# Optimization experiments

Measured on AMD Instinct MI355X. Metric: run time of the kernel, lower is better.

## Reference

```python
import jax, jax.numpy as jnp
import numpy as np

N, E, G = 50000, 800000, 64
IN, HID, H1, H2, OUT = 128, 64, 4, 4, 10
NEG_SLOPE = 0.2


def gat_layer(h, src, dst, W, attn_l, attn_r, bias, n_nodes, n_heads, d):
    # h: [N, F_in] -> feat: [N, H, D]
    feat = (h @ W).reshape(n_nodes, n_heads, d)
    el = jnp.sum(feat * attn_l, axis=-1)          # [N, H]
    er = jnp.sum(feat * attn_r, axis=-1)          # [N, H]
    e = jax.nn.leaky_relu(el[src] + er[dst], NEG_SLOPE)  # [E, H]
    # edge softmax per destination node (numerically stable)
    m = jax.ops.segment_max(e, dst, num_segments=n_nodes)   # [N, H]
    ex = jnp.exp(e - m[dst])                                 # [E, H]
    s = jax.ops.segment_sum(ex, dst, num_segments=n_nodes)   # [N, H]
    alpha = ex / s[dst]                                      # [E, H]
    msg = alpha[:, :, None] * feat[src]                      # [E, H, D]
    out = jax.ops.segment_sum(msg, dst, num_segments=n_nodes)  # [N, H, D]
    return jax.nn.elu(out + bias.reshape(1, n_heads, d))


def setup_inputs() -> dict:
    key = jax.random.key(0)
    ks = jax.random.split(key, 16)
    x = jax.random.normal(ks[0], (N, IN), dtype=jnp.float32)
    src = jax.random.randint(ks[1], (E,), 0, N, dtype=jnp.int32)
    dst = jax.random.randint(ks[2], (E,), 0, N, dtype=jnp.int32)
    graph_ids = jnp.sort(jax.random.randint(ks[3], (N,), 0, G, dtype=jnp.int32))
    sc1 = 1.0 / np.sqrt(IN)
    sc2 = 1.0 / np.sqrt(HID * H1)
    W1 = jax.random.normal(ks[4], (IN, H1 * HID), dtype=jnp.float32) * sc1
    attn_l1 = jax.random.normal(ks[5], (H1, HID), dtype=jnp.float32) * 0.1
    attn_r1 = jax.random.normal(ks[6], (H1, HID), dtype=jnp.float32) * 0.1
    b1 = jnp.zeros((H1 * HID,), dtype=jnp.float32)
    W2 = jax.random.normal(ks[7], (H1 * HID, H2 * HID), dtype=jnp.float32) * sc2
    attn_l2 = jax.random.normal(ks[8], (H2, HID), dtype=jnp.float32) * 0.1
    attn_r2 = jax.random.normal(ks[9], (H2, HID), dtype=jnp.float32) * 0.1
    b2 = jnp.zeros((H2 * HID,), dtype=jnp.float32)
    fcW = jax.random.normal(ks[10], (HID, OUT), dtype=jnp.float32) * (1.0 / np.sqrt(HID))
    fcb = jnp.zeros((OUT,), dtype=jnp.float32)
    return {"x": x, "src": src, "dst": dst, "graph_ids": graph_ids,
            "W1": W1, "attn_l1": attn_l1, "attn_r1": attn_r1, "b1": b1,
            "W2": W2, "attn_l2": attn_l2, "attn_r2": attn_r2, "b2": b2,
            "fcW": fcW, "fcb": fcb}


def reference(x, src, dst, graph_ids, W1, attn_l1, attn_r1, b1,
              W2, attn_l2, attn_r2, b2, fcW, fcb):
    h = gat_layer(x, src, dst, W1, attn_l1, attn_r1, b1, N, H1, HID)
    h = h.reshape(N, H1 * HID)                    # flatten heads (layer 0)
    h = gat_layer(h, src, dst, W2, attn_l2, attn_r2, b2, N, H2, HID)
    h = h.mean(axis=1)                            # mean over heads (layer 1) -> [N, HID]
    pooled = jax.ops.segment_sum(h, graph_ids, num_segments=G)  # SumPooling -> [G, HID]
    return pooled @ fcW + fcb                     # dropout is identity in eval
```

## Files before the change

kernel.cpp:

```cpp
#include <hip/hip_runtime.h>
#include <math.h>

#define NN 50000
#define MPAD 50048
#define NE 800000
#define NG 64
#define FIN 128
#define FH 256
#define HID 64
#define NH 4
#define NOUT 10
#define NEG_SLOPE 0.2f
#define NSB ((NN + 1023) / 1024)

typedef unsigned short u16;
typedef __attribute__((ext_vector_type(8))) short short8;
typedef __attribute__((ext_vector_type(4))) float f32x4;

static __device__ __forceinline__ float leaky(float x){ return x > 0.f ? x : NEG_SLOPE * x; }
static __device__ __forceinline__ float elu1(float x){ return x > 0.f ? x : (__expf(x) - 1.f); }
static __device__ __forceinline__ float b2f(u16 u){
  union { unsigned int i; float f; } v; v.i = ((unsigned)u) << 16; return v.f;
}
static __device__ __forceinline__ u16 f2b(float f){
  union { float f; unsigned int i; } v; v.f = f;
  unsigned r = v.i + 0x7FFFu + ((v.i >> 16) & 1u);
  return (u16)(r >> 16);
}

static __device__ __forceinline__ void gl_lds16(const u16* g, u16* l){
  __builtin_amdgcn_global_load_lds(
      (const __attribute__((address_space(1))) void*)g,
      (__attribute__((address_space(3))) void*)l, 16, 0, 0);
}

#define HIST_BLKS ((NE + 255) / 256)
#define F2B_BLKS (NN * FIN / 4 / 256)
#define W1_BLKS  (FIN * FH / 256)
#define W2_BLKS  (FH * FH / 256)
__global__ void k_histprep(const int* __restrict__ dst, int* __restrict__ cnt,
                           int* __restrict__ rank,
                           const float* __restrict__ x, u16* __restrict__ xh,
                           const float* __restrict__ W1, u16* __restrict__ Wtc1,
                           const float* __restrict__ W2, u16* __restrict__ Wtc2,
                           float* __restrict__ pooled)
{
  int b = blockIdx.x;
  if (b < HIST_BLKS){
    int i = b * 256 + threadIdx.x;
    if (i < NE) rank[i] = atomicAdd(&cnt[dst[i]], 1);
  } else if (b < HIST_BLKS + F2B_BLKS){
    int i = ((b - HIST_BLKS) * 256 + threadIdx.x) * 4;
    float4 v = *reinterpret_cast<const float4*>(x + i);
    ushort4 o; o.x = f2b(v.x); o.y = f2b(v.y); o.z = f2b(v.z); o.w = f2b(v.w);
    *reinterpret_cast<ushort4*>(xh + i) = o;
  } else if (b < HIST_BLKS + F2B_BLKS + W1_BLKS){
    int e = (b - HIST_BLKS - F2B_BLKS) * 256 + threadIdx.x;
    int k = e >> 8, c = e & 255;
    float w = W1[e];
    u16 hi = f2b(w);
    float lo = w - b2f(hi);
    Wtc1[(size_t)c * 2 * FIN + k] = hi;
    Wtc1[(size_t)c * 2 * FIN + FIN + k] = f2b(lo);
  } else if (b < HIST_BLKS + F2B_BLKS + W1_BLKS + W2_BLKS){
    int e = (b - HIST_BLKS - F2B_BLKS - W1_BLKS) * 256 + threadIdx.x;
    int k = e >> 8, c = e & 255;
    float w = W2[e];
    u16 hi = f2b(w);
    float lo = w - b2f(hi);
    Wtc2[(size_t)c * 2 * FH + k] = hi;
    Wtc2[(size_t)c * 2 * FH + FH + k] = f2b(lo);
  } else {
    float4 z = make_float4(0.f, 0.f, 0.f, 0.f);
    #pragma unroll
    for (int l = 0; l < 4; l++)
      *reinterpret_cast<float4*>(pooled + (l * 256 + threadIdx.x) * 4) = z;
  }
}

__global__ __launch_bounds__(256) void k_scan1(const int* __restrict__ cnt,
    int* __restrict__ offs, int* __restrict__ bsum)
{
  __shared__ int wsum[4];
  int t = threadIdx.x;
  int lane = t & 63, wv = t >> 6;
  int base = blockIdx.x * 1024 + t * 4;
  int4 v = make_int4(0, 0, 0, 0);
  if (base + 3 < NN) v = *reinterpret_cast<const int4*>(cnt + base);
  else {
    if (base + 0 < NN) v.x = cnt[base + 0];
    if (base + 1 < NN) v.y = cnt[base + 1];
    if (base + 2 < NN) v.z = cnt[base + 2];
  }
  int s = v.x + v.y + v.z + v.w;
  int incl = s;
  #pragma unroll
  for (int d = 1; d < 64; d <<= 1){
    int u = __shfl_up(incl, d);
    if (lane >= d) incl += u;
  }
  if (lane == 63) wsum[wv] = incl;
  __syncthreads();
  int woff = 0;
  #pragma unroll
  for (int i = 0; i < 4; i++) if (i < wv) woff += wsum[i];
  int texcl = woff + incl - s;
  int e0 = texcl, e1 = e0 + v.x, e2 = e1 + v.y, e3 = e2 + v.z;
  if (base + 3 < NN) *reinterpret_cast<int4*>(offs + base) = make_int4(e0, e1, e2, e3);
  else {
    if (base + 0 < NN) offs[base + 0] = e0;
    if (base + 1 < NN) offs[base + 1] = e1;
    if (base + 2 < NN) offs[base + 2] = e2;
  }
  if (t == 255) bsum[blockIdx.x] = woff + incl;
}

__global__ void k_scan2(const int* __restrict__ bsum, int* __restrict__ bpre)
{
  int lane = threadIdx.x;
  int s = (lane < NSB) ? bsum[lane] : 0;
  int incl = s;
  #pragma unroll
  for (int d = 1; d < 64; d <<= 1){
    int u = __shfl_up(incl, d);
    if (lane >= d) incl += u;
  }
  if (lane < NSB) bpre[lane] = incl - s;
}

__global__ void k_scatter(const int* __restrict__ src, const int* __restrict__ dst,
                          const int* __restrict__ offs, const int* __restrict__ bpre,
                          const int* __restrict__ rank, int* __restrict__ csrc){
  int i = blockIdx.x * blockDim.x + threadIdx.x;
  if (i < NE){
    int d = dst[i];
    csrc[offs[d] + bpre[d >> 10] + rank[i]] = src[i];
  }
}

template<int K>
__global__ __launch_bounds__(512) void k_gemm_bf(
    const u16* __restrict__ A, const u16* __restrict__ Wtc, u16* __restrict__ C,
    const float* __restrict__ attn_l, const float* __restrict__ attn_r,
    float* __restrict__ el, float* __restrict__ er)
{
  constexpr int K2 = 2 * K;
  __shared__ union {
    struct { u16 a[128 * 32]; u16 b[256 * 32]; } s;
    u16 ct[128 * 256];
  } L;
  int t = threadIdx.x;
  int wv = t >> 6, lane = t & 63;
  int row0 = blockIdx.x * 128;
  int lr = lane & 15, lk = lane >> 4;
  int wm = wv >> 2, wn = wv & 3;

  f32x4 acc[4][4];
  #pragma unroll
  for (int m = 0; m < 4; m++)
    #pragma unroll
    for (int n = 0; n < 4; n++) acc[m][n] = (f32x4){0.f, 0.f, 0.f, 0.f};

  const u16* asrc = A + (size_t)(row0 + wv * 16 + (lane >> 2)) * K + (lane & 3) * 8;
  u16* aldst = &L.s.a[wv * 512];
  const u16* bsrc0 = Wtc + (size_t)(wv * 32 + (lane >> 2)) * K2 + (lane & 3) * 8;
  const u16* bsrc1 = Wtc + (size_t)(wv * 32 + 16 + (lane >> 2)) * K2 + (lane & 3) * 8;
  u16* bldst0 = &L.s.b[wv * 1024];
  u16* bldst1 = &L.s.b[wv * 1024 + 512];

  for (int k0 = 0; k0 < K2; k0 += 32){
    int acol = k0 & (K - 1);
    gl_lds16(asrc + acol, aldst);
    gl_lds16(bsrc0 + k0, bldst0);
    gl_lds16(bsrc1 + k0, bldst1);
    __syncthreads();
    short8 af[4], bf[4];
    #pragma unroll
    for (int m = 0; m < 4; m++)
      af[m] = *reinterpret_cast<const short8*>(&L.s.a[(wm * 64 + m * 16 + lr) * 32 + lk * 8]);
    #pragma unroll
    for (int n = 0; n < 4; n++)
      bf[n] = *reinterpret_cast<const short8*>(&L.s.b[(wn * 64 + n * 16 + lr) * 32 + lk * 8]);
    #pragma unroll
    for (int m = 0; m < 4; m++)
      #pragma unroll
      for (int n = 0; n < 4; n++)
        acc[m][n] = __builtin_amdgcn_mfma_f32_16x16x32_bf16(af[m], bf[n], acc[m][n], 0, 0, 0);
    __syncthreads();
  }

  int rg = lane >> 4;
  #pragma unroll
  for (int m = 0; m < 4; m++)
    #pragma unroll
    for (int n = 0; n < 4; n++)
      #pragma unroll
      for (int r = 0; r < 4; r++)
        L.ct[(wm * 64 + m * 16 + rg * 4 + r) * 256 + wn * 64 + n * 16 + lr] = f2b(acc[m][n][r]);
  __syncthreads();
  #pragma unroll
  for (int l = 0; l < 8; l++){
    int idx = t + l * 512;
    int row = idx >> 5, colg = idx & 31;
    short8 v = *reinterpret_cast<const short8*>(&L.ct[row * 256 + colg * 8]);
    *reinterpret_cast<short8*>(C + (size_t)(row0 + row) * 256 + colg * 8) = v;
  }

  {
    int r = t >> 2, hh = t & 3;
    const u16* crow = &L.ct[r * 256 + hh * 64];
    float pl = 0.f, pr = 0.f;
    #pragma unroll
    for (int d8 = 0; d8 < 8; d8++){
      short8 cv = *reinterpret_cast<const short8*>(crow + d8 * 8);
      const float* alp = &attn_l[hh * 64 + d8 * 8];
      const float* arp = &attn_r[hh * 64 + d8 * 8];
      #pragma unroll
      for (int q = 0; q < 8; q++){
        float fv = b2f((u16)cv[q]);
        pl = fmaf(fv, alp[q], pl);
        pr = fmaf(fv, arp[q], pr);
      }
    }
    int orow = row0 + r;
    el[orow * 4 + hh] = pl;
    er[orow * 4 + hh] = pr;
  }
}

template<int LAYER>
__global__ __launch_bounds__(256) void k_agg2(const u16* __restrict__ feat,
    const float* __restrict__ el, const float* __restrict__ er,
    const int* __restrict__ offs, const int* __restrict__ bpre,
    const int* __restrict__ cnt, const int* __restrict__ csrc,
    const float* __restrict__ bias, void* __restrict__ outv)
{
  int wv = threadIdx.x >> 6, lane = threadIdx.x & 63;
  int n = blockIdx.x * 4 + wv;
  if (n >= NN) return;
  int e0 = offs[n] + bpre[n >> 10];
  int deg = cnt[n];
  int hs = lane & 3, slot = lane >> 2;
  int ha = lane >> 4;
  float erh = er[n * 4 + hs];

  float m = -1e30f, srun = 0.f;
  float a0 = 0.f, a1 = 0.f, a2 = 0.f, a3 = 0.f;

  for (int base = 0; base < deg; base += 16){
    int cntc = min(16, deg - base);
    int idx = base + slot;
    int sj = 0; float v = -1e30f;
    if (idx < deg){
      sj = csrc[e0 + idx];
      v = leaky(el[sj * 4 + hs] + erh);
    }
    float cmax = v;
    #pragma unroll
    for (int d = 4; d < 64; d <<= 1) cmax = fmaxf(cmax, __shfl_xor(cmax, d));
    float nm = fmaxf(m, cmax);
    float fac = __expf(m - nm);
    float ex = __expf(v - nm);
    float csum = ex;
    #pragma unroll
    for (int d = 4; d < 64; d <<= 1) csum += __shfl_xor(csum, d);
    srun = srun * fac + csum;
    m = nm;
    float fa = __shfl(fac, ha);
    a0 *= fa; a1 *= fa; a2 *= fa; a3 *= fa;
    #pragma unroll 4
    for (int jj = 0; jj < cntc; jj++){
      float w = __shfl(ex, jj * 4 + ha);
      int sjj = __shfl(sj, jj * 4);
      ushort4 fv = *reinterpret_cast<const ushort4*>(feat + (size_t)sjj * FH + lane * 4);
      a0 = fmaf(w, b2f(fv.x), a0);
      a1 = fmaf(w, b2f(fv.y), a1);
      a2 = fmaf(w, b2f(fv.z), a2);
      a3 = fmaf(w, b2f(fv.w), a3);
    }
  }

  float invh = (deg > 0) ? 1.f / srun : 0.f;
  float inv = __shfl(invh, ha);
  float4 bv = *reinterpret_cast<const float4*>(&bias[lane * 4]);
  a0 = elu1(a0 * inv + bv.x); a1 = elu1(a1 * inv + bv.y);
  a2 = elu1(a2 * inv + bv.z); a3 = elu1(a3 * inv + bv.w);

  if (LAYER == 1){
    u16* out = (u16*)outv;
    ushort4 o; o.x = f2b(a0); o.y = f2b(a1); o.z = f2b(a2); o.w = f2b(a3);
    *reinterpret_cast<ushort4*>(out + (size_t)n * FH + lane * 4) = o;
  } else {
    float* out = (float*)outv;
    a0 += __shfl_xor(a0, 16); a0 += __shfl_xor(a0, 32);
    a1 += __shfl_xor(a1, 16); a1 += __shfl_xor(a1, 32);
    a2 += __shfl_xor(a2, 16); a2 += __shfl_xor(a2, 32);
    a3 += __shfl_xor(a3, 16); a3 += __shfl_xor(a3, 32);
    if (lane < 16){
      float4 o = make_float4(a0 * 0.25f, a1 * 0.25f, a2 * 0.25f, a3 * 0.25f);
      *reinterpret_cast<float4*>(out + (size_t)n * HID + lane * 4) = o;
    }
  }
}

__global__ __launch_bounds__(256) void k_pool(const float* __restrict__ h2,
    const int* __restrict__ gid, float* __restrict__ pooled)
{
  int wv = threadIdx.x >> 6, lane = threadIdx.x & 63;
  int w = blockIdx.x * 4 + wv;
  int base = w * 64;
  if (base >= NN) return;
  int grp = lane >> 4, c4 = (lane & 15) * 4;
  int curg = -1;
  float4 acc = make_float4(0.f, 0.f, 0.f, 0.f);
  #pragma unroll 4
  for (int it = 0; it < 16; it++){
    int row = base + it * 4 + grp;
    if (row >= NN) break;
    int g = gid[row];
    if (g != curg){
      if (curg >= 0){
        atomicAdd(&pooled[curg * HID + c4 + 0], acc.x);
        atomicAdd(&pooled[curg * HID + c4 + 1], acc.y);
        atomicAdd(&pooled[curg * HID + c4 + 2], acc.z);
        atomicAdd(&pooled[curg * HID + c4 + 3], acc.w);
      }
      curg = g; acc = make_float4(0.f, 0.f, 0.f, 0.f);
    }
    float4 v = *reinterpret_cast<const float4*>(&h2[(size_t)row * HID + c4]);
    acc.x += v.x; acc.y += v.y; acc.z += v.z; acc.w += v.w;
  }
  if (curg >= 0){
    atomicAdd(&pooled[curg * HID + c4 + 0], acc.x);
    atomicAdd(&pooled[curg * HID + c4 + 1], acc.y);
    atomicAdd(&pooled[curg * HID + c4 + 2], acc.z);
    atomicAdd(&pooled[curg * HID + c4 + 3], acc.w);
  }
}

__global__ void k_fc(const float* __restrict__ pooled, const float* __restrict__ fcW,
                     const float* __restrict__ fcb, float* __restrict__ out)
{
  int t = threadIdx.x;
  if (t >= NG * NOUT) return;
  int g = t / NOUT, o = t % NOUT;
  float s = fcb[o];
  for (int d = 0; d < HID; d++) s = fmaf(pooled[g * HID + d], fcW[d * NOUT + o], s);
  out[t] = s;
}

static inline size_t align_up(size_t x){ return (x + 255) & ~(size_t)255; }

extern "C" void kernel_launch(void* const* d_in, const int* in_sizes, int n_in,
                              void* d_out, int out_size, void* d_ws, size_t ws_size,
                              hipStream_t stream) {
  const float* x    = (const float*)d_in[0];
  const int*   src  = (const int*)d_in[1];
  const int*   dst  = (const int*)d_in[2];
  const int*   gid  = (const int*)d_in[3];
  const float* W1   = (const float*)d_in[4];
  const float* al1  = (const float*)d_in[5];
  const float* ar1  = (const float*)d_in[6];
  const float* b1   = (const float*)d_in[7];
  const float* W2   = (const float*)d_in[8];
  const float* al2  = (const float*)d_in[9];
  const float* ar2  = (const float*)d_in[10];
  const float* b2   = (const float*)d_in[11];
  const float* fcW  = (const float*)d_in[12];
  const float* fcb  = (const float*)d_in[13];
  float* out = (float*)d_out;

  char* p = (char*)d_ws;
  int* cnt  = (int*)p; p += align_up((size_t)NN * 4);
  int* offs = (int*)p; p += align_up((size_t)NN * 4);
  int* bsum = (int*)p; p += align_up((size_t)NSB * 4);
  int* bpre = (int*)p; p += align_up((size_t)NSB * 4);
  int* rank = (int*)p; p += align_up((size_t)NE * 4);
  int* csrc = (int*)p; p += align_up((size_t)NE * 4);
  u16* xh    = (u16*)p; p += align_up((size_t)MPAD * FIN * 2);
  u16* feath = (u16*)p; p += align_up((size_t)MPAD * FH * 2);
  u16* h1h   = (u16*)p; p += align_up((size_t)MPAD * FH * 2);
  float* elb = (float*)p; p += align_up((size_t)MPAD * NH * 4);
  float* erb = (float*)p; p += align_up((size_t)MPAD * NH * 4);
  float* h2  = (float*)p; p += align_up((size_t)NN * HID * 4);
  float* pooled = (float*)p; p += align_up((size_t)NG * HID * 4);
  u16* Wtc1 = (u16*)p; p += align_up((size_t)FIN * FH * 2 * 2);
  u16* Wtc2 = (u16*)p; p += align_up((size_t)FH * FH * 2 * 2);

  hipMemsetAsync(cnt, 0, (size_t)NN * 4, stream);

  const int EB = (NE + 255) / 256;
  const int NB4 = (NN + 3) / 4;
  const int GB = MPAD / 128;
  const int HP = HIST_BLKS + F2B_BLKS + W1_BLKS + W2_BLKS + 1;

  k_histprep<<<HP, 256, 0, stream>>>(dst, cnt, rank, x, xh, W1, Wtc1, W2, Wtc2, pooled);
  k_scan1<<<NSB, 256, 0, stream>>>(cnt, offs, bsum);
  k_scan2<<<1, 64, 0, stream>>>(bsum, bpre);
  k_scatter<<<EB, 256, 0, stream>>>(src, dst, offs, bpre, rank, csrc);

  k_gemm_bf<FIN><<<GB, 512, 0, stream>>>(xh, Wtc1, feath, al1, ar1, elb, erb);
  k_agg2<1><<<NB4, 256, 0, stream>>>(feath, elb, erb, offs, bpre, cnt, csrc, b1, h1h);

  k_gemm_bf<FH><<<GB, 512, 0, stream>>>(h1h, Wtc2, feath, al2, ar2, elb, erb);
  k_agg2<2><<<NB4, 256, 0, stream>>>(feath, elb, erb, offs, bpre, cnt, csrc, b2, h2);

  k_pool<<<(NN + 255) / 256, 256, 0, stream>>>(h2, gid, pooled);
  k_fc<<<1, 640, 0, stream>>>(pooled, fcW, fcb, out);
}
```

Before: 301.4 us.

## Fold block-prefix scan into consumers and gather two edges per wave with 16-byte loads

The separate single-wave kernel that scans the per-block sums is removed. Each consumer block (scatter and both aggregations) now recomputes that 64-entry prefix into shared memory, trading a launch and a dependency for redundant tiny work per block. The aggregation kernel now splits each wave into two halves that handle alternating edges, with each lane loading 8 bf16 values in one 16-byte load. The halves are combined with a cross-half shuffle at the end, which halves the serial gather iterations per node but doubles the accumulator registers. The early `n >= NN` return was dropped so the barrier is safe; NN is a multiple of 4 here, so no out-of-range nodes occur.

```diff
diff --git a/kernel.cpp b/kernel.cpp
--- a/kernel.cpp
+++ b/kernel.cpp
@@ -115,26 +115,33 @@
   if (t == 255) bsum[blockIdx.x] = woff + incl;
 }
 
-__global__ void k_scan2(const int* __restrict__ bsum, int* __restrict__ bpre)
-{
-  int lane = threadIdx.x;
-  int s = (lane < NSB) ? bsum[lane] : 0;
-  int incl = s;
-  #pragma unroll
-  for (int d = 1; d < 64; d <<= 1){
-    int u = __shfl_up(incl, d);
-    if (lane >= d) incl += u;
-  }
-  if (lane < NSB) bpre[lane] = incl - s;
-}
-
-__global__ void k_scatter(const int* __restrict__ src, const int* __restrict__ dst,
-                          const int* __restrict__ offs, const int* __restrict__ bpre,
-                          const int* __restrict__ rank, int* __restrict__ csrc){
+static __device__ __forceinline__ void block_bpre(const int* __restrict__ bsum,
+                                                  int* sb)
+{
+  int t = threadIdx.x;
+  if (t < 64){
+    int s = (t < NSB) ? bsum[t] : 0;
+    int incl = s;
+    #pragma unroll
+    for (int d = 1; d < 64; d <<= 1){
+      int u = __shfl_up(incl, d);
+      if (t >= d) incl += u;
+    }
+    sb[t] = incl - s;
+  }
+  __syncthreads();
+}
+
+__global__ __launch_bounds__(256) void k_scatter(const int* __restrict__ src,
+    const int* __restrict__ dst, const int* __restrict__ offs,
+    const int* __restrict__ bsum, const int* __restrict__ rank,
+    int* __restrict__ csrc){
+  __shared__ int sb[64];
+  block_bpre(bsum, sb);
   int i = blockIdx.x * blockDim.x + threadIdx.x;
   if (i < NE){
     int d = dst[i];
-    csrc[offs[d] + bpre[d >> 10] + rank[i]] = src[i];
+    csrc[offs[d] + sb[d >> 10] + rank[i]] = src[i];
   }
 }
 
@@ -231,21 +238,25 @@
 template<int LAYER>
 __global__ __launch_bounds__(256) void k_agg2(const u16* __restrict__ feat,
     const float* __restrict__ el, const float* __restrict__ er,
-    const int* __restrict__ offs, const int* __restrict__ bpre,
+    const int* __restrict__ offs, const int* __restrict__ bsum,
     const int* __restrict__ cnt, const int* __restrict__ csrc,
     const float* __restrict__ bias, void* __restrict__ outv)
 {
+  __shared__ int sb[64];
+  block_bpre(bsum, sb);
   int wv = threadIdx.x >> 6, lane = threadIdx.x & 63;
   int n = blockIdx.x * 4 + wv;
-  if (n >= NN) return;
-  int e0 = offs[n] + bpre[n >> 10];
+  int e0 = offs[n] + sb[n >> 10];
   int deg = cnt[n];
   int hs = lane & 3, slot = lane >> 2;
-  int ha = lane >> 4;
+  int half = lane >> 5, k = lane & 31;
+  int hk = k >> 3;
   float erh = er[n * 4 + hs];
 
   float m = -1e30f, srun = 0.f;
-  float a0 = 0.f, a1 = 0.f, a2 = 0.f, a3 = 0.f;
+  float a[8];
+  #pragma unroll
+  for (int p = 0; p < 8; p++) a[p] = 0.f;
 
   for (int base = 0; base < deg; base += 16){
     int cntc = min(16, deg - base);
@@ -266,39 +277,54 @@
     for (int d = 4; d < 64; d <<= 1) csum += __shfl_xor(csum, d);
     srun = srun * fac + csum;
     m = nm;
-    float fa = __shfl(fac, ha);
-    a0 *= fa; a1 *= fa; a2 *= fa; a3 *= fa;
-    #pragma unroll 4
-    for (int jj = 0; jj < cntc; jj++){
-      float w = __shfl(ex, jj * 4 + ha);
-      int sjj = __shfl(sj, jj * 4);
-      ushort4 fv = *reinterpret_cast<const ushort4*>(feat + (size_t)sjj * FH + lane * 4);
-      a0 = fmaf(w, b2f(fv.x), a0);
-      a1 = fmaf(w, b2f(fv.y), a1);
-      a2 = fmaf(w, b2f(fv.z), a2);
-      a3 = fmaf(w, b2f(fv.w), a3);
+    float fa = __shfl(fac, hk);
+    #pragma unroll
+    for (int p = 0; p < 8; p++) a[p] *= fa;
+    int jjmax = (cntc + 1) >> 1;
+    for (int jj = 0; jj < jjmax; jj++){
+      int e = jj * 2 + half;
+      float w = __shfl(ex, e * 4 + hk);
+      int sjj = __shfl(sj, e * 4);
+      short8 fv = *reinterpret_cast<const short8*>(feat + (size_t)sjj * FH + k * 8);
+      #pragma unroll
+      for (int p = 0; p < 8; p++) a[p] = fmaf(w, b2f((u16)fv[p]), a[p]);
     }
   }
 
   float invh = (deg > 0) ? 1.f / srun : 0.f;
-  float inv = __shfl(invh, ha);
-  float4 bv = *reinterpret_cast<const float4*>(&bias[lane * 4]);
-  a0 = elu1(a0 * inv + bv.x); a1 = elu1(a1 * inv + bv.y);
-  a2 = elu1(a2 * inv + bv.z); a3 = elu1(a3 * inv + bv.w);
+  float inv = __shfl(invh, hk);
+  #pragma unroll
+  for (int p = 0; p < 8; p++) a[p] += __shfl_xor(a[p], 32);
+
+  float4 bv0 = *reinterpret_cast<const float4*>(&bias[k * 8]);
+  float4 bv1 = *reinterpret_cast<const float4*>(&bias[k * 8 + 4]);
+  float ev[8];
+  ev[0] = elu1(a[0] * inv + bv0.x); ev[1] = elu1(a[1] * inv + bv0.y);
+  ev[2] = elu1(a[2] * inv + bv0.z); ev[3] = elu1(a[3] * inv + bv0.w);
+  ev[4] = elu1(a[4] * inv + bv1.x); ev[5] = elu1(a[5] * inv + bv1.y);
+  ev[6] = elu1(a[6] * inv + bv1.z); ev[7] = elu1(a[7] * inv + bv1.w);
 
   if (LAYER == 1){
-    u16* out = (u16*)outv;
-    ushort4 o; o.x = f2b(a0); o.y = f2b(a1); o.z = f2b(a2); o.w = f2b(a3);
-    *reinterpret_cast<ushort4*>(out + (size_t)n * FH + lane * 4) = o;
+    if (lane < 32){
+      u16* out = (u16*)outv;
+      short8 o;
+      #pragma unroll
+      for (int p = 0; p < 8; p++) o[p] = (short)f2b(ev[p]);
+      *reinterpret_cast<short8*>(out + (size_t)n * FH + k * 8) = o;
+    }
   } else {
-    float* out = (float*)outv;
-    a0 += __shfl_xor(a0, 16); a0 += __shfl_xor(a0, 32);
-    a1 += __shfl_xor(a1, 16); a1 += __shfl_xor(a1, 32);
-    a2 += __shfl_xor(a2, 16); a2 += __shfl_xor(a2, 32);
-    a3 += __shfl_xor(a3, 16); a3 += __shfl_xor(a3, 32);
-    if (lane < 16){
-      float4 o = make_float4(a0 * 0.25f, a1 * 0.25f, a2 * 0.25f, a3 * 0.25f);
-      *reinterpret_cast<float4*>(out + (size_t)n * HID + lane * 4) = o;
+    #pragma unroll
+    for (int p = 0; p < 8; p++){
+      ev[p] += __shfl_xor(ev[p], 8);
+      ev[p] += __shfl_xor(ev[p], 16);
+      ev[p] *= 0.25f;
+    }
+    if (lane < 8){
+      float* out = (float*)outv;
+      float4 o0 = make_float4(ev[0], ev[1], ev[2], ev[3]);
+      float4 o1 = make_float4(ev[4], ev[5], ev[6], ev[7]);
+      *reinterpret_cast<float4*>(out + (size_t)n * HID + lane * 8) = o0;
+      *reinterpret_cast<float4*>(out + (size_t)n * HID + lane * 8 + 4) = o1;
     }
   }
 }
@@ -374,7 +400,6 @@
   int* cnt  = (int*)p; p += align_up((size_t)NN * 4);
   int* offs = (int*)p; p += align_up((size_t)NN * 4);
   int* bsum = (int*)p; p += align_up((size_t)NSB * 4);
-  int* bpre = (int*)p; p += align_up((size_t)NSB * 4);
   int* rank = (int*)p; p += align_up((size_t)NE * 4);
   int* csrc = (int*)p; p += align_up((size_t)NE * 4);
   u16* xh    = (u16*)p; p += align_up((size_t)MPAD * FIN * 2);
@@ -396,14 +421,13 @@
 
   k_histprep<<<HP, 256, 0, stream>>>(dst, cnt, rank, x, xh, W1, Wtc1, W2, Wtc2, pooled);
   k_scan1<<<NSB, 256, 0, stream>>>(cnt, offs, bsum);
-  k_scan2<<<1, 64, 0, stream>>>(bsum, bpre);
-  k_scatter<<<EB, 256, 0, stream>>>(src, dst, offs, bpre, rank, csrc);
+  k_scatter<<<EB, 256, 0, stream>>>(src, dst, offs, bsum, rank, csrc);
 
   k_gemm_bf<FIN><<<GB, 512, 0, stream>>>(xh, Wtc1, feath, al1, ar1, elb, erb);
-  k_agg2<1><<<NB4, 256, 0, stream>>>(feath, elb, erb, offs, bpre, cnt, csrc, b1, h1h);
+  k_agg2<1><<<NB4, 256, 0, stream>>>(feath, elb, erb, offs, bsum, cnt, csrc, b1, h1h);
 
   k_gemm_bf<FH><<<GB, 512, 0, stream>>>(h1h, Wtc2, feath, al2, ar2, elb, erb);
-  k_agg2<2><<<NB4, 256, 0, stream>>>(feath, elb, erb, offs, bpre, cnt, csrc, b2, h2);
+  k_agg2<2><<<NB4, 256, 0, stream>>>(feath, elb, erb, offs, bsum, cnt, csrc, b2, h2);
 
   k_pool<<<(NN + 255) / 256, 256, 0, stream>>>(h2, gid, pooled);
   k_fc<<<1, 640, 0, stream>>>(pooled, fcW, fcb, out);
```

Measured after the change: 285.6 us. 1.06x faster.
